# Performance work log

Measured on AMD Instinct MI355X. Metric: run time of the kernel, lower is better.

The kernel has to match this reference:

```python
import jax, jax.numpy as jnp
import numpy as np

D_MODEL = 768
N_HEAD = 12
D_KEY = D_MODEL // N_HEAD  # 64
B, S = 2, 1024


def setup_inputs() -> dict:
    key = jax.random.key(0)
    ks = jax.random.split(key, 13)
    f = jax.random.normal
    scale = 1.0 / np.sqrt(D_MODEL)
    return {
        "queries": f(ks[0], (B, S, D_MODEL), jnp.float32),
        "keys": f(ks[1], (B, S, D_MODEL), jnp.float32),
        "values": f(ks[2], (B, S, D_MODEL), jnp.float32),
        "relation_k": f(ks[3], (B, S, S, D_KEY), jnp.float32),
        "relation_v": f(ks[4], (B, S, S, D_KEY), jnp.float32),
        "Wq": f(ks[5], (D_MODEL, D_MODEL), jnp.float32) * scale,
        "bq": jnp.zeros((D_MODEL,), jnp.float32),
        "Wk": f(ks[6], (D_MODEL, D_MODEL), jnp.float32) * scale,
        "bk": jnp.zeros((D_MODEL,), jnp.float32),
        "Wv": f(ks[7], (D_MODEL, D_MODEL), jnp.float32) * scale,
        "bv": jnp.zeros((D_MODEL,), jnp.float32),
        "Wo": f(ks[8], (D_MODEL, D_MODEL), jnp.float32) * scale,
        "bo": jnp.zeros((D_MODEL,), jnp.float32),
    }


def _split_heads(x):
    # [B, S, H*D] -> [B, H, S, D]
    b, s, _ = x.shape
    return x.reshape(b, s, N_HEAD, -1).transpose(0, 2, 1, 3)


def reference(queries, keys, values, relation_k, relation_v,
              Wq, bq, Wk, bk, Wv, bv, Wo, bo):
    q = _split_heads(queries @ Wq + bq)
    k = _split_heads(keys @ Wk + bk)
    v = _split_heads(values @ Wv + bv)

    # module scales q by d_key^-0.5 BEFORE logits, which divide by sqrt(d_key)
    # again -> effective 1/d_key scaling (faithful to source)
    q = q * (D_KEY ** -0.5)

    qk = jnp.einsum("bhqd,bhkd->bhqk", q, k)
    q_rel = jnp.einsum("bhqd,bqkd->bhqk", q, relation_k)
    scores = (qk + q_rel) / jnp.sqrt(jnp.float32(D_KEY))

    probs = jax.nn.softmax(scores, axis=-1)  # dropout omitted (eval mode)

    wv = jnp.einsum("bhqk,bhkd->bhqd", probs, v)
    w_rel = jnp.einsum("bhqk,bqkd->bhqd", probs, relation_v)
    out = wv + w_rel  # [B, H, S, D]

    out = out.transpose(0, 2, 1, 3).reshape(queries.shape[0], queries.shape[1], -1)
    return out @ Wo + bo
```

## Files before the change

### kernel.cpp

```cpp
#include <hip/hip_runtime.h>
#include <hip/hip_bf16.h>

#define BATCH 2
#define SEQ   1024
#define DM    768
#define NH    12
#define DK    64

#define OFF_QS    0
#define OFF_KS    1572864
#define OFF_VS    3145728
#define OFF_ATTN  4718592
#define OFF_SC    6291456

__global__ __launch_bounds__(256) void gemm_bias_kernel(
    const float* __restrict__ X, const float* __restrict__ W,
    const float* __restrict__ bias, float* __restrict__ C, float alpha)
{
    __shared__ float As[16][65];
    __shared__ float Bs[16][65];
    const int bm = blockIdx.x, bn = blockIdx.y;
    const int tid = threadIdx.x;
    const int tx = tid & 15, ty = tid >> 4;
    float acc[4][4] = {};
    for (int kt = 0; kt < DM; kt += 16) {
        __syncthreads();
#pragma unroll
        for (int l = 0; l < 4; ++l) {
            int idx = tid + l * 256;
            int m = idx >> 4, kk = idx & 15;
            As[kk][m] = X[(bm * 64 + m) * DM + kt + kk];
        }
#pragma unroll
        for (int l = 0; l < 4; ++l) {
            int idx = tid + l * 256;
            int kk = idx >> 6, n = idx & 63;
            Bs[kk][n] = W[(kt + kk) * DM + bn * 64 + n];
        }
        __syncthreads();
#pragma unroll
        for (int kk = 0; kk < 16; ++kk) {
            float a[4], bb[4];
#pragma unroll
            for (int i = 0; i < 4; ++i) a[i] = As[kk][ty * 4 + i];
#pragma unroll
            for (int j = 0; j < 4; ++j) bb[j] = Bs[kk][tx * 4 + j];
#pragma unroll
            for (int i = 0; i < 4; ++i)
#pragma unroll
                for (int j = 0; j < 4; ++j) acc[i][j] += a[i] * bb[j];
        }
    }
#pragma unroll
    for (int i = 0; i < 4; ++i) {
        int row = bm * 64 + ty * 4 + i;
#pragma unroll
        for (int j = 0; j < 4; ++j) {
            int col = bn * 64 + tx * 4 + j;
            C[row * DM + col] = alpha * (acc[i][j] + bias[col]);
        }
    }
}

__global__ __launch_bounds__(256) void qk_kernel(
    const float* __restrict__ qs, const float* __restrict__ ks,
    float* __restrict__ scores)
{
    const int kt = blockIdx.x, qt = blockIdx.y, bh = blockIdx.z;
    const int b = bh / NH, h = bh % NH;
    __shared__ float Qs[64][65];
    __shared__ float Ks[64][65];
    const int tid = threadIdx.x;
#pragma unroll
    for (int l = 0; l < 16; ++l) {
        int idx = tid + l * 256;
        int m = idx >> 6, d = idx & 63;
        Qs[m][d] = qs[(b * SEQ + qt * 64 + m) * DM + h * 64 + d];
        Ks[m][d] = ks[(b * SEQ + kt * 64 + m) * DM + h * 64 + d];
    }
    __syncthreads();
    const int tx = tid & 15, ty = tid >> 4;
    float acc[4][4] = {};
#pragma unroll 8
    for (int d = 0; d < 64; ++d) {
        float a[4], bb[4];
#pragma unroll
        for (int i = 0; i < 4; ++i) a[i] = Qs[ty * 4 + i][d];
#pragma unroll
        for (int j = 0; j < 4; ++j) bb[j] = Ks[tx * 4 + j][d];
#pragma unroll
        for (int i = 0; i < 4; ++i)
#pragma unroll
            for (int j = 0; j < 4; ++j) acc[i][j] += a[i] * bb[j];
    }
#pragma unroll
    for (int i = 0; i < 4; ++i) {
        int q = qt * 64 + ty * 4 + i;
#pragma unroll
        for (int j = 0; j < 4; ++j) {
            int k = kt * 64 + tx * 4 + j;
            scores[((size_t)bh * SEQ + q) * SEQ + k] = acc[i][j];
        }
    }
}

__global__ __launch_bounds__(256) void relk_kernel(
    const float* __restrict__ qs, const float* __restrict__ rk,
    float* __restrict__ scores)
{
    const int kc = blockIdx.x, q = blockIdx.y, b = blockIdx.z;
    __shared__ float qv[DM];
    __shared__ float Rs[64][65];
    const int tid = threadIdx.x;
    if (tid < 192) {
        float4 t = *(const float4*)&qs[(b * SEQ + q) * DM + tid * 4];
        *(float4*)&qv[tid * 4] = t;
    }
    const int k = tid & 63;
    const int hb = tid >> 6;
    const size_t rbase = ((size_t)(b * SEQ + q)) * SEQ * DK;
    for (int sub = 0; sub < 4; ++sub) {
        const int k0 = kc * 256 + sub * 64;
        __syncthreads();
#pragma unroll
        for (int l = 0; l < 16; ++l) {
            int idx = tid + l * 256;
            int kk = idx >> 6, d = idx & 63;
            Rs[kk][d] = rk[rbase + (size_t)(k0 + kk) * DK + d];
        }
        __syncthreads();
        float a0 = 0.f, a1 = 0.f, a2 = 0.f;
#pragma unroll 8
        for (int d = 0; d < 64; ++d) {
            float r = Rs[k][d];
            a0 += r * qv[hb * 64 + d];
            a1 += r * qv[(hb + 4) * 64 + d];
            a2 += r * qv[(hb + 8) * 64 + d];
        }
        size_t s0 = ((size_t)(b * NH + hb) * SEQ + q) * SEQ + k0 + k;
        scores[s0] += a0;
        scores[s0 + (size_t)4 * SEQ * SEQ] += a1;
        scores[s0 + (size_t)8 * SEQ * SEQ] += a2;
    }
}

__global__ __launch_bounds__(256) void softmax_kernel(float* __restrict__ scores)
{
    const int row = blockIdx.x;
    float* p = scores + (size_t)row * SEQ;
    const int tid = threadIdx.x;
    float4 x = *(float4*)&p[tid * 4];
    float m = fmaxf(fmaxf(x.x, x.y), fmaxf(x.z, x.w));
#pragma unroll
    for (int off = 32; off > 0; off >>= 1) m = fmaxf(m, __shfl_xor(m, off));
    __shared__ float redm[4], reds[4];
    if ((tid & 63) == 0) redm[tid >> 6] = m;
    __syncthreads();
    m = fmaxf(fmaxf(redm[0], redm[1]), fmaxf(redm[2], redm[3]));
    float e0 = __expf(x.x - m), e1 = __expf(x.y - m);
    float e2 = __expf(x.z - m), e3 = __expf(x.w - m);
    float s = e0 + e1 + e2 + e3;
#pragma unroll
    for (int off = 32; off > 0; off >>= 1) s += __shfl_xor(s, off);
    if ((tid & 63) == 0) reds[tid >> 6] = s;
    __syncthreads();
    float inv = 1.0f / (reds[0] + reds[1] + reds[2] + reds[3]);
    x.x = e0 * inv; x.y = e1 * inv; x.z = e2 * inv; x.w = e3 * inv;
    *(float4*)&p[tid * 4] = x;
}

__global__ __launch_bounds__(256) void wv_kernel(
    const float* __restrict__ scores, const float* __restrict__ vs,
    float* __restrict__ attn)
{
    const int qt = blockIdx.x, bh = blockIdx.y;
    const int b = bh / NH, h = bh % NH;
    __shared__ float Ps[64][65];
    __shared__ float Vs[64][65];
    const int tid = threadIdx.x;
    const int tx = tid & 15, ty = tid >> 4;
    float acc[4][4] = {};
    for (int kt = 0; kt < 16; ++kt) {
        __syncthreads();
#pragma unroll
        for (int l = 0; l < 16; ++l) {
            int idx = tid + l * 256;
            int m = idx >> 6, d = idx & 63;
            Ps[m][d] = scores[((size_t)bh * SEQ + qt * 64 + m) * SEQ + kt * 64 + d];
            Vs[m][d] = vs[(b * SEQ + kt * 64 + m) * DM + h * 64 + d];
        }
        __syncthreads();
#pragma unroll 8
        for (int kk = 0; kk < 64; ++kk) {
            float a[4], bb[4];
#pragma unroll
            for (int i = 0; i < 4; ++i) a[i] = Ps[ty * 4 + i][kk];
#pragma unroll
            for (int j = 0; j < 4; ++j) bb[j] = Vs[kk][tx * 4 + j];
#pragma unroll
            for (int i = 0; i < 4; ++i)
#pragma unroll
                for (int j = 0; j < 4; ++j) acc[i][j] += a[i] * bb[j];
        }
    }
#pragma unroll
    for (int i = 0; i < 4; ++i) {
        int q = qt * 64 + ty * 4 + i;
#pragma unroll
        for (int j = 0; j < 4; ++j) {
            int d = tx * 4 + j;
            attn[(b * SEQ + q) * DM + h * 64 + d] = acc[i][j];
        }
    }
}

__global__ __launch_bounds__(256) void wrel_kernel(
    const float* __restrict__ scores, const float* __restrict__ rv,
    float* __restrict__ attn)
{
    const int q = blockIdx.x, b = blockIdx.y;
    __shared__ float Ps[12][68];
    __shared__ float RVs[64][65];
    const int tid = threadIdx.x;
    const int d = tid & 63, hb = tid >> 6;
    const size_t rbase = ((size_t)(b * SEQ + q)) * SEQ * DK;
    float a0 = 0.f, a1 = 0.f, a2 = 0.f;
    for (int kt = 0; kt < 16; ++kt) {
        __syncthreads();
        if (tid < 192) {
            int h = tid >> 4, j = tid & 15;
            float4 t = *(const float4*)&scores[((size_t)(b * NH + h) * SEQ + q) * SEQ + kt * 64 + j * 4];
            *(float4*)&Ps[h][j * 4] = t;
        }
#pragma unroll
        for (int l = 0; l < 16; ++l) {
            int idx = tid + l * 256;
            int kk = idx >> 6, dd = idx & 63;
            RVs[kk][dd] = rv[rbase + (size_t)(kt * 64 + kk) * DK + dd];
        }
        __syncthreads();
#pragma unroll 8
        for (int kk = 0; kk < 64; ++kk) {
            float r = RVs[kk][d];
            a0 += Ps[hb][kk] * r;
            a1 += Ps[hb + 4][kk] * r;
            a2 += Ps[hb + 8][kk] * r;
        }
    }
    float* ap = attn + (size_t)(b * SEQ + q) * DM;
    ap[hb * 64 + d] += a0;
    ap[(hb + 4) * 64 + d] += a1;
    ap[(hb + 8) * 64 + d] += a2;
}

extern "C" void kernel_launch(void* const* d_in, const int* in_sizes, int n_in,
                              void* d_out, int out_size, void* d_ws, size_t ws_size,
                              hipStream_t stream)
{
    const float* queries = (const float*)d_in[0];
    const float* keys    = (const float*)d_in[1];
    const float* values  = (const float*)d_in[2];
    const float* rk      = (const float*)d_in[3];
    const float* rv      = (const float*)d_in[4];
    const float* Wq      = (const float*)d_in[5];
    const float* bq      = (const float*)d_in[6];
    const float* Wk      = (const float*)d_in[7];
    const float* bk      = (const float*)d_in[8];
    const float* Wv      = (const float*)d_in[9];
    const float* bv      = (const float*)d_in[10];
    const float* Wo      = (const float*)d_in[11];
    const float* bo      = (const float*)d_in[12];
    float* out = (float*)d_out;
    float* ws  = (float*)d_ws;

    float* qs    = ws + OFF_QS;
    float* ks    = ws + OFF_KS;
    float* vs    = ws + OFF_VS;
    float* attn  = ws + OFF_ATTN;
    float* sc    = ws + OFF_SC;

    dim3 gblk(256);
    dim3 ggrid(32, 12);
    hipLaunchKernelGGL(gemm_bias_kernel, ggrid, gblk, 0, stream, queries, Wq, bq, qs, 1.0f / 64.0f);
    hipLaunchKernelGGL(gemm_bias_kernel, ggrid, gblk, 0, stream, keys,    Wk, bk, ks, 1.0f);
    hipLaunchKernelGGL(gemm_bias_kernel, ggrid, gblk, 0, stream, values,  Wv, bv, vs, 1.0f);
    hipLaunchKernelGGL(qk_kernel,   dim3(16, 16, 24), gblk, 0, stream, qs, ks, sc);
    hipLaunchKernelGGL(relk_kernel, dim3(4, 1024, 2), gblk, 0, stream, qs, rk, sc);
    hipLaunchKernelGGL(softmax_kernel, dim3(24576), gblk, 0, stream, sc);
    hipLaunchKernelGGL(wv_kernel,   dim3(16, 24),   gblk, 0, stream, sc, vs, attn);
    hipLaunchKernelGGL(wrel_kernel, dim3(1024, 2),  gblk, 0, stream, sc, rv, attn);
    hipLaunchKernelGGL(gemm_bias_kernel, ggrid, gblk, 0, stream, attn, Wo, bo, out, 1.0f);
}
```

Baseline: 1.764 ms.

## Rewrite GEMM and attention kernels to use wave-uniform scalar broadcast loads

The shared-memory tiled GEMM, QK and PV kernels are replaced with per-wave register-accumulation loops. Each wave handles 16 rows, and the row operand (X, Q, P) is read by wave-uniform float4 loads that can go through the scalar path. The relk and wrel kernels now load relation tiles with float4 and read q or probabilities straight from global memory with uniform addresses instead of staging them in LDS. The intent is to cut LDS traffic and barriers and to widen loads, at the cost of less data reuse across lanes and more reliance on the cache.

```diff
diff --git a/kernel.cpp b/kernel.cpp
--- a/kernel.cpp
+++ b/kernel.cpp
@@ -1,5 +1,4 @@
 #include <hip/hip_runtime.h>
-#include <hip/hip_bf16.h>
 
 #define BATCH 2
 #define SEQ   1024
@@ -17,49 +16,32 @@
     const float* __restrict__ X, const float* __restrict__ W,
     const float* __restrict__ bias, float* __restrict__ C, float alpha)
 {
-    __shared__ float As[16][65];
-    __shared__ float Bs[16][65];
     const int bm = blockIdx.x, bn = blockIdx.y;
     const int tid = threadIdx.x;
-    const int tx = tid & 15, ty = tid >> 4;
-    float acc[4][4] = {};
-    for (int kt = 0; kt < DM; kt += 16) {
-        __syncthreads();
-#pragma unroll
-        for (int l = 0; l < 4; ++l) {
-            int idx = tid + l * 256;
-            int m = idx >> 4, kk = idx & 15;
-            As[kk][m] = X[(bm * 64 + m) * DM + kt + kk];
-        }
-#pragma unroll
-        for (int l = 0; l < 4; ++l) {
-            int idx = tid + l * 256;
-            int kk = idx >> 6, n = idx & 63;
-            Bs[kk][n] = W[(kt + kk) * DM + bn * 64 + n];
-        }
-        __syncthreads();
-#pragma unroll
-        for (int kk = 0; kk < 16; ++kk) {
-            float a[4], bb[4];
-#pragma unroll
-            for (int i = 0; i < 4; ++i) a[i] = As[kk][ty * 4 + i];
-#pragma unroll
-            for (int j = 0; j < 4; ++j) bb[j] = Bs[kk][tx * 4 + j];
-#pragma unroll
-            for (int i = 0; i < 4; ++i)
-#pragma unroll
-                for (int j = 0; j < 4; ++j) acc[i][j] += a[i] * bb[j];
-        }
-    }
-#pragma unroll
-    for (int i = 0; i < 4; ++i) {
-        int row = bm * 64 + ty * 4 + i;
-#pragma unroll
-        for (int j = 0; j < 4; ++j) {
-            int col = bn * 64 + tx * 4 + j;
-            C[row * DM + col] = alpha * (acc[i][j] + bias[col]);
-        }
-    }
+    const int lane = tid & 63;
+    const int wid = __builtin_amdgcn_readfirstlane(tid >> 6);
+    const int col = bn * 64 + lane;
+    const float* xrow = X + (size_t)(bm * 64 + wid * 16) * DM;
+    const float* wcol = W + col;
+    float acc[16] = {};
+    for (int k4 = 0; k4 < DM; k4 += 4) {
+        float w0 = wcol[(size_t)(k4 + 0) * DM];
+        float w1 = wcol[(size_t)(k4 + 1) * DM];
+        float w2 = wcol[(size_t)(k4 + 2) * DM];
+        float w3 = wcol[(size_t)(k4 + 3) * DM];
+#pragma unroll
+        for (int r = 0; r < 16; ++r) {
+            float4 x4 = *(const float4*)&xrow[(size_t)r * DM + k4];
+            acc[r] = fmaf(x4.x, w0, acc[r]);
+            acc[r] = fmaf(x4.y, w1, acc[r]);
+            acc[r] = fmaf(x4.z, w2, acc[r]);
+            acc[r] = fmaf(x4.w, w3, acc[r]);
+        }
+    }
+    const float bcol = bias[col];
+    float* crow = C + (size_t)(bm * 64 + wid * 16) * DM + col;
+#pragma unroll
+    for (int r = 0; r < 16; ++r) crow[(size_t)r * DM] = alpha * (acc[r] + bcol);
 }
 
 __global__ __launch_bounds__(256) void qk_kernel(
@@ -68,39 +50,40 @@
 {
     const int kt = blockIdx.x, qt = blockIdx.y, bh = blockIdx.z;
     const int b = bh / NH, h = bh % NH;
-    __shared__ float Qs[64][65];
-    __shared__ float Ks[64][65];
-    const int tid = threadIdx.x;
-#pragma unroll
-    for (int l = 0; l < 16; ++l) {
+    __shared__ float Kt[64][65];
+    const int tid = threadIdx.x;
+    const int lane = tid & 63;
+    const int wid = __builtin_amdgcn_readfirstlane(tid >> 6);
+#pragma unroll
+    for (int l = 0; l < 4; ++l) {
         int idx = tid + l * 256;
-        int m = idx >> 6, d = idx & 63;
-        Qs[m][d] = qs[(b * SEQ + qt * 64 + m) * DM + h * 64 + d];
-        Ks[m][d] = ks[(b * SEQ + kt * 64 + m) * DM + h * 64 + d];
+        int m = idx >> 4, d4 = idx & 15;
+        float4 t = *(const float4*)&ks[(size_t)(b * SEQ + kt * 64 + m) * DM + h * 64 + d4 * 4];
+        Kt[d4 * 4 + 0][m] = t.x;
+        Kt[d4 * 4 + 1][m] = t.y;
+        Kt[d4 * 4 + 2][m] = t.z;
+        Kt[d4 * 4 + 3][m] = t.w;
     }
     __syncthreads();
-    const int tx = tid & 15, ty = tid >> 4;
-    float acc[4][4] = {};
-#pragma unroll 8
-    for (int d = 0; d < 64; ++d) {
-        float a[4], bb[4];
-#pragma unroll
-        for (int i = 0; i < 4; ++i) a[i] = Qs[ty * 4 + i][d];
-#pragma unroll
-        for (int j = 0; j < 4; ++j) bb[j] = Ks[tx * 4 + j][d];
-#pragma unroll
-        for (int i = 0; i < 4; ++i)
-#pragma unroll
-            for (int j = 0; j < 4; ++j) acc[i][j] += a[i] * bb[j];
-    }
-#pragma unroll
-    for (int i = 0; i < 4; ++i) {
-        int q = qt * 64 + ty * 4 + i;
-#pragma unroll
-        for (int j = 0; j < 4; ++j) {
-            int k = kt * 64 + tx * 4 + j;
-            scores[((size_t)bh * SEQ + q) * SEQ + k] = acc[i][j];
-        }
+    float kreg[64];
+#pragma unroll
+    for (int d = 0; d < 64; ++d) kreg[d] = Kt[d][lane];
+
+    const float* qbase = qs + (size_t)(b * SEQ + qt * 64 + wid * 16) * DM + h * 64;
+    float* srow = scores + ((size_t)bh * SEQ + qt * 64 + wid * 16) * SEQ + kt * 64 + lane;
+#pragma unroll 4
+    for (int r = 0; r < 16; ++r) {
+        const float* qr = qbase + (size_t)r * DM;
+        float a0 = 0.f, a1 = 0.f, a2 = 0.f, a3 = 0.f;
+#pragma unroll
+        for (int dq = 0; dq < 16; ++dq) {
+            float4 q4 = *(const float4*)&qr[dq * 4];
+            a0 = fmaf(q4.x, kreg[dq * 4 + 0], a0);
+            a1 = fmaf(q4.y, kreg[dq * 4 + 1], a1);
+            a2 = fmaf(q4.z, kreg[dq * 4 + 2], a2);
+            a3 = fmaf(q4.w, kreg[dq * 4 + 3], a3);
+        }
+        srow[(size_t)r * SEQ] = (a0 + a1) + (a2 + a3);
     }
 }
 
@@ -109,33 +92,39 @@
     float* __restrict__ scores)
 {
     const int kc = blockIdx.x, q = blockIdx.y, b = blockIdx.z;
-    __shared__ float qv[DM];
     __shared__ float Rs[64][65];
     const int tid = threadIdx.x;
-    if (tid < 192) {
-        float4 t = *(const float4*)&qs[(b * SEQ + q) * DM + tid * 4];
-        *(float4*)&qv[tid * 4] = t;
-    }
     const int k = tid & 63;
-    const int hb = tid >> 6;
+    const int hb = __builtin_amdgcn_readfirstlane(tid >> 6);
+    const float* qrow = qs + (size_t)(b * SEQ + q) * DM;
     const size_t rbase = ((size_t)(b * SEQ + q)) * SEQ * DK;
     for (int sub = 0; sub < 4; ++sub) {
         const int k0 = kc * 256 + sub * 64;
         __syncthreads();
 #pragma unroll
-        for (int l = 0; l < 16; ++l) {
+        for (int l = 0; l < 4; ++l) {
             int idx = tid + l * 256;
-            int kk = idx >> 6, d = idx & 63;
-            Rs[kk][d] = rk[rbase + (size_t)(k0 + kk) * DK + d];
+            int kk = idx >> 4, d4 = idx & 15;
+            float4 t = *(const float4*)&rk[rbase + (size_t)(k0 + kk) * DK + d4 * 4];
+            Rs[kk][d4 * 4 + 0] = t.x;
+            Rs[kk][d4 * 4 + 1] = t.y;
+            Rs[kk][d4 * 4 + 2] = t.z;
+            Rs[kk][d4 * 4 + 3] = t.w;
         }
         __syncthreads();
         float a0 = 0.f, a1 = 0.f, a2 = 0.f;
-#pragma unroll 8
-        for (int d = 0; d < 64; ++d) {
-            float r = Rs[k][d];
-            a0 += r * qv[hb * 64 + d];
-            a1 += r * qv[(hb + 4) * 64 + d];
-            a2 += r * qv[(hb + 8) * 64 + d];
+#pragma unroll
+        for (int dq = 0; dq < 16; ++dq) {
+            float4 q0 = *(const float4*)&qrow[(hb    ) * 64 + dq * 4];
+            float4 q1 = *(const float4*)&qrow[(hb + 4) * 64 + dq * 4];
+            float4 q2 = *(const float4*)&qrow[(hb + 8) * 64 + dq * 4];
+            float r0 = Rs[k][dq * 4 + 0];
+            float r1 = Rs[k][dq * 4 + 1];
+            float r2 = Rs[k][dq * 4 + 2];
+            float r3 = Rs[k][dq * 4 + 3];
+            a0 = fmaf(r0, q0.x, fmaf(r1, q0.y, fmaf(r2, q0.z, fmaf(r3, q0.w, a0))));
+            a1 = fmaf(r0, q1.x, fmaf(r1, q1.y, fmaf(r2, q1.z, fmaf(r3, q1.w, a1))));
+            a2 = fmaf(r0, q2.x, fmaf(r1, q2.y, fmaf(r2, q2.z, fmaf(r3, q2.w, a2))));
         }
         size_t s0 = ((size_t)(b * NH + hb) * SEQ + q) * SEQ + k0 + k;
         scores[s0] += a0;
@@ -175,43 +164,29 @@
 {
     const int qt = blockIdx.x, bh = blockIdx.y;
     const int b = bh / NH, h = bh % NH;
-    __shared__ float Ps[64][65];
-    __shared__ float Vs[64][65];
-    const int tid = threadIdx.x;
-    const int tx = tid & 15, ty = tid >> 4;
-    float acc[4][4] = {};
-    for (int kt = 0; kt < 16; ++kt) {
-        __syncthreads();
-#pragma unroll
-        for (int l = 0; l < 16; ++l) {
-            int idx = tid + l * 256;
-            int m = idx >> 6, d = idx & 63;
-            Ps[m][d] = scores[((size_t)bh * SEQ + qt * 64 + m) * SEQ + kt * 64 + d];
-            Vs[m][d] = vs[(b * SEQ + kt * 64 + m) * DM + h * 64 + d];
-        }
-        __syncthreads();
-#pragma unroll 8
-        for (int kk = 0; kk < 64; ++kk) {
-            float a[4], bb[4];
-#pragma unroll
-            for (int i = 0; i < 4; ++i) a[i] = Ps[ty * 4 + i][kk];
-#pragma unroll
-            for (int j = 0; j < 4; ++j) bb[j] = Vs[kk][tx * 4 + j];
-#pragma unroll
-            for (int i = 0; i < 4; ++i)
-#pragma unroll
-                for (int j = 0; j < 4; ++j) acc[i][j] += a[i] * bb[j];
-        }
-    }
-#pragma unroll
-    for (int i = 0; i < 4; ++i) {
-        int q = qt * 64 + ty * 4 + i;
-#pragma unroll
-        for (int j = 0; j < 4; ++j) {
-            int d = tx * 4 + j;
-            attn[(b * SEQ + q) * DM + h * 64 + d] = acc[i][j];
-        }
-    }
+    const int tid = threadIdx.x;
+    const int lane = tid & 63;
+    const int wid = __builtin_amdgcn_readfirstlane(tid >> 6);
+    const float* prow = scores + ((size_t)bh * SEQ + qt * 64 + wid * 16) * SEQ;
+    const float* vcol = vs + (size_t)b * SEQ * DM + h * 64 + lane;
+    float acc[16] = {};
+    for (int k4 = 0; k4 < SEQ; k4 += 4) {
+        float v0 = vcol[(size_t)(k4 + 0) * DM];
+        float v1 = vcol[(size_t)(k4 + 1) * DM];
+        float v2 = vcol[(size_t)(k4 + 2) * DM];
+        float v3 = vcol[(size_t)(k4 + 3) * DM];
+#pragma unroll
+        for (int r = 0; r < 16; ++r) {
+            float4 p4 = *(const float4*)&prow[(size_t)r * SEQ + k4];
+            acc[r] = fmaf(p4.x, v0, acc[r]);
+            acc[r] = fmaf(p4.y, v1, acc[r]);
+            acc[r] = fmaf(p4.z, v2, acc[r]);
+            acc[r] = fmaf(p4.w, v3, acc[r]);
+        }
+    }
+    float* arow = attn + (size_t)(b * SEQ + qt * 64 + wid * 16) * DM + h * 64 + lane;
+#pragma unroll
+    for (int r = 0; r < 16; ++r) arow[(size_t)r * DM] = acc[r];
 }
 
 __global__ __launch_bounds__(256) void wrel_kernel(
@@ -219,38 +194,46 @@
     float* __restrict__ attn)
 {
     const int q = blockIdx.x, b = blockIdx.y;
-    __shared__ float Ps[12][68];
     __shared__ float RVs[64][65];
     const int tid = threadIdx.x;
-    const int d = tid & 63, hb = tid >> 6;
+    const int d = tid & 63;
+    const int hb = __builtin_amdgcn_readfirstlane(tid >> 6);
     const size_t rbase = ((size_t)(b * SEQ + q)) * SEQ * DK;
+    const float* p0 = scores + ((size_t)(b * NH + hb    ) * SEQ + q) * SEQ;
+    const float* p1 = scores + ((size_t)(b * NH + hb + 4) * SEQ + q) * SEQ;
+    const float* p2 = scores + ((size_t)(b * NH + hb + 8) * SEQ + q) * SEQ;
     float a0 = 0.f, a1 = 0.f, a2 = 0.f;
     for (int kt = 0; kt < 16; ++kt) {
         __syncthreads();
-        if (tid < 192) {
-            int h = tid >> 4, j = tid & 15;
-            float4 t = *(const float4*)&scores[((size_t)(b * NH + h) * SEQ + q) * SEQ + kt * 64 + j * 4];
-            *(float4*)&Ps[h][j * 4] = t;
-        }
-#pragma unroll
-        for (int l = 0; l < 16; ++l) {
+#pragma unroll
+        for (int l = 0; l < 4; ++l) {
             int idx = tid + l * 256;
-            int kk = idx >> 6, dd = idx & 63;
-            RVs[kk][dd] = rv[rbase + (size_t)(kt * 64 + kk) * DK + dd];
-        }
-        __syncthreads();
-#pragma unroll 8
-        for (int kk = 0; kk < 64; ++kk) {
-            float r = RVs[kk][d];
-            a0 += Ps[hb][kk] * r;
-            a1 += Ps[hb + 4][kk] * r;
-            a2 += Ps[hb + 8][kk] * r;
-        }
-    }
-    float* ap = attn + (size_t)(b * SEQ + q) * DM;
-    ap[hb * 64 + d] += a0;
-    ap[(hb + 4) * 64 + d] += a1;
-    ap[(hb + 8) * 64 + d] += a2;
+            int kk = idx >> 4, d4 = idx & 15;
+            float4 t = *(const float4*)&rv[rbase + (size_t)(kt * 64 + kk) * DK + d4 * 4];
+            RVs[kk][d4 * 4 + 0] = t.x;
+            RVs[kk][d4 * 4 + 1] = t.y;
+            RVs[kk][d4 * 4 + 2] = t.z;
+            RVs[kk][d4 * 4 + 3] = t.w;
+        }
+        __syncthreads();
+#pragma unroll
+        for (int k4 = 0; k4 < 16; ++k4) {
+            float4 P0 = *(const float4*)&p0[kt * 64 + k4 * 4];
+            float4 P1 = *(const float4*)&p1[kt * 64 + k4 * 4];
+            float4 P2 = *(const float4*)&p2[kt * 64 + k4 * 4];
+            float r0 = RVs[k4 * 4 + 0][d];
+            float r1 = RVs[k4 * 4 + 1][d];
+            float r2 = RVs[k4 * 4 + 2][d];
+            float r3 = RVs[k4 * 4 + 3][d];
+            a0 = fmaf(P0.x, r0, fmaf(P0.y, r1, fmaf(P0.z, r2, fmaf(P0.w, r3, a0))));
+            a1 = fmaf(P1.x, r0, fmaf(P1.y, r1, fmaf(P1.z, r2, fmaf(P1.w, r3, a1))));
+            a2 = fmaf(P2.x, r0, fmaf(P2.y, r1, fmaf(P2.z, r2, fmaf(P2.w, r3, a2))));
+        }
+    }
+    float* ap = attn + (size_t)(b * SEQ + q) * DM + d;
+    ap[(hb    ) * 64] += a0;
+    ap[(hb + 4) * 64] += a1;
+    ap[(hb + 8) * 64] += a2;
 }
 
 extern "C" void kernel_launch(void* const* d_in, const int* in_sizes, int n_in,
```

New measurement: 2.188 ms. 1.24x slower.
